# Optimization experiments

Measured on AMD Instinct MI355X. Metric: run time of the kernel, lower is better.

Reference implementation:

```python
import jax, jax.numpy as jnp
import numpy as np

NUM_CATEGORIES = 64
INPUT_DIM = 256
HIDDEN_DIM = 256
N = 4096  # number of samples (each with its own category)
M = 16    # rows per sample


def setup_inputs() -> dict:
    key = jax.random.key(0)
    k_x, k_cat, k_W = jax.random.split(key, 3)
    x = jax.random.normal(k_x, (N, M, INPUT_DIM), dtype=jnp.float32)
    cat_ids = jax.random.randint(k_cat, (N,), 0, NUM_CATEGORIES, dtype=jnp.int64)
    W = 0.02 * jax.random.normal(k_W, (NUM_CATEGORIES, INPUT_DIM, HIDDEN_DIM), dtype=jnp.float32)
    b = jnp.zeros((NUM_CATEGORIES, HIDDEN_DIM), dtype=jnp.float32)
    return {"x": x, "cat_ids": cat_ids, "W": W, "b": b}


def reference(x, cat_ids, W, b):
    # Gather per-sample weights/biases, then batched matmul + bias add.
    selected_W = W[cat_ids]              # [N, input_dim, hidden_dim]
    selected_b = b[cat_ids]              # [N, hidden_dim]
    out = jnp.einsum('nmi,nih->nmh', x, selected_W) + selected_b[:, None, :]
    return out
```

## Files before the change

### kernel.cpp

```cpp
#include <hip/hip_runtime.h>
#include <hip/hip_bf16.h>
#include <stdint.h>

#define N_SAMPLES 4096
#define M_ROWS 16
#define K_DIM 256
#define H_DIM 256
#define N_CATS 64
#define SPB 4
#define MAX_PADDED (N_SAMPLES + N_CATS * (SPB - 1))
#define NGROUP (MAX_PADDED / SPB)
#define GPX (NGROUP / 8)
#define GEMM_GRID (NGROUP * 2)

typedef _Float16 half8 __attribute__((ext_vector_type(8)));
typedef float floatx4 __attribute__((ext_vector_type(4)));

#define WT_BYTES ((size_t)N_CATS * K_DIM * H_DIM * 2)
#define ORD_OFF  WT_BYTES
#define WS_NEED  (ORD_OFF + (size_t)MAX_PADDED * 4)

__global__ __launch_bounds__(256)
void prep_combined(const float* __restrict__ W, _Float16* __restrict__ Wt,
                   const int* __restrict__ cat, int* __restrict__ ord) {
  const int tid = threadIdx.x;
  if (blockIdx.x < 1024) {
    __shared__ _Float16 t[64][72];
    const int bid = blockIdx.x;
    const int c  = bid >> 4;
    const int kb = (bid >> 2) & 3;
    const int hb = bid & 3;
    const int r  = tid >> 2;
    const int cg = (tid & 3) * 16;
    const float* src = W + ((size_t)c << 16) + (size_t)(kb * 64 + r) * 256 + hb * 64 + cg;
#pragma unroll
    for (int j = 0; j < 16; j += 4) {
      float4 v = *(const float4*)(src + j);
      t[r][cg + j + 0] = (_Float16)v.x;
      t[r][cg + j + 1] = (_Float16)v.y;
      t[r][cg + j + 2] = (_Float16)v.z;
      t[r][cg + j + 3] = (_Float16)v.w;
    }
    __syncthreads();
    _Float16* dst = Wt + ((size_t)c << 16) + (size_t)(hb * 64 + r) * 256 + kb * 64 + cg;
    half8 o0, o1;
#pragma unroll
    for (int j = 0; j < 8; j++) o0[j] = t[cg + j][r];
#pragma unroll
    for (int j = 0; j < 8; j++) o1[j] = t[cg + 8 + j][r];
    *(half8*)(dst) = o0;
    *(half8*)(dst + 8) = o1;
  } else {
    __shared__ int hist[N_CATS];
    __shared__ int poffs[N_CATS];
    __shared__ int curs[N_CATS];
    if (tid < N_CATS) hist[tid] = 0;
    for (int i = tid; i < MAX_PADDED; i += 256) ord[i] = -1;
    __syncthreads();
    for (int i = tid; i < N_SAMPLES; i += 256) atomicAdd(&hist[cat[i]], 1);
    __syncthreads();
    if (tid == 0) {
      int run = 0;
      for (int c = 0; c < N_CATS; c++) {
        poffs[c] = run;
        run += ((hist[c] + SPB - 1) / SPB) * SPB;
      }
    }
    if (tid < N_CATS) curs[tid] = 0;
    __syncthreads();
    for (int i = tid; i < N_SAMPLES; i += 256) {
      int c = cat[i];
      int p = poffs[c] + atomicAdd(&curs[c], 1);
      ord[p] = i;
    }
  }
}

__global__ __launch_bounds__(256, 8)
void gemm_kernel(const float* __restrict__ x, const int* __restrict__ cat_ids,
                 const float* __restrict__ bias, const _Float16* __restrict__ Wt,
                 const int* __restrict__ ord, float* __restrict__ out) {
  __shared__ _Float16 sA[64 * 32];
  __shared__ _Float16 sB[128 * 32];
  __shared__ int s_meta[SPB];

  const int tid = threadIdx.x;
  const int B = blockIdx.x;
  const int xcd = B & 7;
  const int slot = B >> 3;
  const int h_half = slot & 1;
  const int group = xcd * GPX + (slot >> 1);
  const int h0 = h_half << 7;

  if (tid < SPB) s_meta[tid] = ord[group * SPB + tid];
  __syncthreads();
  const int s0 = s_meta[0];
  if (s0 < 0) return;
  const int cat = cat_ids[s0];

  const int wid  = tid >> 6;
  const int lane = tid & 63;
  const int l15  = lane & 15;
  const int quad = lane >> 4;

  const int arow = tid >> 2;
  const int akq  = tid & 3;
  const int asmp = s_meta[arow >> 4];
  const float* asrc = (asmp >= 0)
      ? (x + ((size_t)asmp * 16 + (arow & 15)) * K_DIM + akq * 8) : nullptr;
  _Float16* adst = &sA[arow * 32 + akq * 8];

  const _Float16* wbase = Wt + ((size_t)cat << 16);

  floatx4 acc[4][2];
#pragma unroll
  for (int i = 0; i < 4; i++)
#pragma unroll
    for (int j = 0; j < 2; j++)
#pragma unroll
      for (int e = 0; e < 4; e++) acc[i][j][e] = 0.0f;

  for (int kt = 0; kt < K_DIM / 32; ++kt) {
    __syncthreads();
    if (asrc) {
      const float4* p = (const float4*)(asrc + kt * 32);
      float4 v0 = p[0], v1 = p[1];
      half8 h;
      h[0] = (_Float16)v0.x; h[1] = (_Float16)v0.y;
      h[2] = (_Float16)v0.z; h[3] = (_Float16)v0.w;
      h[4] = (_Float16)v1.x; h[5] = (_Float16)v1.y;
      h[6] = (_Float16)v1.z; h[7] = (_Float16)v1.w;
      *(half8*)adst = h;
    } else {
      half8 h;
#pragma unroll
      for (int j = 0; j < 8; j++) h[j] = (_Float16)0.0f;
      *(half8*)adst = h;
    }
#pragma unroll
    for (int j = 0; j < 2; j++) {
      const int hloc = wid * 16 + 64 * j;
      const _Float16* g = wbase + (size_t)(h0 + hloc + (lane >> 2)) * K_DIM + kt * 32 + (lane & 3) * 8;
      __builtin_amdgcn_global_load_lds(
          (__attribute__((address_space(1))) void*)g,
          (__attribute__((address_space(3))) void*)&sB[hloc * 32], 16, 0, 0);
    }
    __syncthreads();
    half8 af[4], bf[2];
#pragma unroll
    for (int mt = 0; mt < 4; mt++)
      af[mt] = *(const half8*)&sA[(mt * 16 + l15) * 32 + quad * 8];
#pragma unroll
    for (int nt = 0; nt < 2; nt++)
      bf[nt] = *(const half8*)&sB[(wid * 32 + nt * 16 + l15) * 32 + quad * 8];
#pragma unroll
    for (int mt = 0; mt < 4; mt++)
#pragma unroll
      for (int nt = 0; nt < 2; nt++)
        acc[mt][nt] = __builtin_amdgcn_mfma_f32_16x16x32_f16(af[mt], bf[nt], acc[mt][nt], 0, 0, 0);
  }

#pragma unroll
  for (int mt = 0; mt < 4; mt++) {
    int s = s_meta[mt];
    if (s < 0) continue;
    float* obase = out + (size_t)s * 16 * H_DIM;
#pragma unroll
    for (int nt = 0; nt < 2; nt++) {
      int col = h0 + wid * 32 + nt * 16 + l15;
      float bv = bias[cat * H_DIM + col];
#pragma unroll
      for (int r = 0; r < 4; r++) {
        int row = quad * 4 + r;
        obase[(size_t)row * H_DIM + col] = acc[mt][nt][r] + bv;
      }
    }
  }
}

__global__ __launch_bounds__(256)
void naive_kernel(const float* __restrict__ x, const int* __restrict__ cat,
                  const float* __restrict__ W, const float* __restrict__ bias,
                  float* __restrict__ out) {
  __shared__ float sx[16 * 256];
  const int n = blockIdx.x;
  const int tid = threadIdx.x;
  const int c = cat[n];
  const float* xs = x + (size_t)n * 16 * 256;
  for (int i = tid; i < 16 * 256; i += 256) sx[i] = xs[i];
  __syncthreads();
  const float* Wc = W + ((size_t)c << 16);
  float accv[16];
  float bv = bias[c * 256 + tid];
#pragma unroll
  for (int m = 0; m < 16; m++) accv[m] = bv;
  for (int k = 0; k < 256; k++) {
    float w = Wc[(size_t)k * 256 + tid];
#pragma unroll
    for (int m = 0; m < 16; m++) accv[m] += sx[m * 256 + k] * w;
  }
#pragma unroll
  for (int m = 0; m < 16; m++) out[((size_t)n * 16 + m) * 256 + tid] = accv[m];
}

extern "C" void kernel_launch(void* const* d_in, const int* in_sizes, int n_in,
                              void* d_out, int out_size, void* d_ws, size_t ws_size,
                              hipStream_t stream) {
  const float* x    = (const float*)d_in[0];
  const int*   cat  = (const int*)d_in[1];
  const float* W    = (const float*)d_in[2];
  const float* bias = (const float*)d_in[3];
  float* out = (float*)d_out;

  if (ws_size < WS_NEED) {
    naive_kernel<<<N_SAMPLES, 256, 0, stream>>>(x, cat, W, bias, out);
    return;
  }

  char* ws = (char*)d_ws;
  _Float16* Wt = (_Float16*)ws;
  int* ord = (int*)(ws + ORD_OFF);

  prep_combined<<<1025, 256, 0, stream>>>(W, Wt, cat, ord);
  gemm_kernel<<<GEMM_GRID, 256, 0, stream>>>(x, cat, bias, Wt, ord, out);
}
```

Measured before the change: 176.6 us.

## Stage full-K A tile in LDS and load B fragments directly to registers

Replaces the 8-step K loop, which had two barriers per step, with a single upfront load. The whole 64x256 fp16 A tile goes into padded LDS (row stride 264) with all x loads in flight at once. Each wave loads its B fragments for all K straight from global into registers, dropping the B LDS staging. Only one barrier remains before the MFMA loop. In exchange it uses more LDS and registers (launch bounds lowered to 4 waves per SIMD), so occupancy may fall.

Result: faster. 169.5 us (-4.0%).

```diff
diff --git a/kernel.cpp b/kernel.cpp
--- a/kernel.cpp
+++ b/kernel.cpp
@@ -12,6 +12,7 @@
 #define NGROUP (MAX_PADDED / SPB)
 #define GPX (NGROUP / 8)
 #define GEMM_GRID (NGROUP * 2)
+#define AROW_STRIDE 264
 
 typedef _Float16 half8 __attribute__((ext_vector_type(8)));
 typedef float floatx4 __attribute__((ext_vector_type(4)));
@@ -76,12 +77,11 @@
   }
 }
 
-__global__ __launch_bounds__(256, 8)
+__global__ __launch_bounds__(256, 4)
 void gemm_kernel(const float* __restrict__ x, const int* __restrict__ cat_ids,
                  const float* __restrict__ bias, const _Float16* __restrict__ Wt,
                  const int* __restrict__ ord, float* __restrict__ out) {
-  __shared__ _Float16 sA[64 * 32];
-  __shared__ _Float16 sB[128 * 32];
+  __shared__ _Float16 sA[64 * AROW_STRIDE];
   __shared__ int s_meta[SPB];
 
   const int tid = threadIdx.x;
@@ -103,14 +103,43 @@
   const int l15  = lane & 15;
   const int quad = lane >> 4;
 
-  const int arow = tid >> 2;
-  const int akq  = tid & 3;
-  const int asmp = s_meta[arow >> 4];
-  const float* asrc = (asmp >= 0)
-      ? (x + ((size_t)asmp * 16 + (arow & 15)) * K_DIM + akq * 8) : nullptr;
-  _Float16* adst = &sA[arow * 32 + akq * 8];
+  const int r = tid >> 2;
+  const int q = tid & 3;
+  const int smp = s_meta[r >> 4];
+  const float* asrc = (smp >= 0)
+      ? (x + ((size_t)smp * 16 + (r & 15)) * K_DIM + q * 64) : nullptr;
+  _Float16* adst = &sA[r * AROW_STRIDE];
+
+#pragma unroll
+  for (int hf = 0; hf < 2; hf++) {
+    float4 v[8];
+    if (asrc) {
+#pragma unroll
+      for (int j = 0; j < 8; j++) v[j] = ((const float4*)asrc)[hf * 8 + j];
+    } else {
+#pragma unroll
+      for (int j = 0; j < 8; j++) v[j] = make_float4(0.f, 0.f, 0.f, 0.f);
+    }
+#pragma unroll
+    for (int oj = 0; oj < 4; oj++) {
+      half8 h;
+      h[0] = (_Float16)v[oj * 2].x;     h[1] = (_Float16)v[oj * 2].y;
+      h[2] = (_Float16)v[oj * 2].z;     h[3] = (_Float16)v[oj * 2].w;
+      h[4] = (_Float16)v[oj * 2 + 1].x; h[5] = (_Float16)v[oj * 2 + 1].y;
+      h[6] = (_Float16)v[oj * 2 + 1].z; h[7] = (_Float16)v[oj * 2 + 1].w;
+      *(half8*)&adst[(q * 8 + hf * 4 + oj) * 8] = h;
+    }
+  }
 
   const _Float16* wbase = Wt + ((size_t)cat << 16);
+  half8 bf[8][2];
+#pragma unroll
+  for (int kt = 0; kt < 8; kt++)
+#pragma unroll
+    for (int nt = 0; nt < 2; nt++) {
+      const int col = h0 + wid * 32 + nt * 16 + l15;
+      bf[kt][nt] = *(const half8*)(wbase + (size_t)col * K_DIM + kt * 32 + quad * 8);
+    }
 
   floatx4 acc[4][2];
 #pragma unroll
@@ -120,46 +149,25 @@
 #pragma unroll
       for (int e = 0; e < 4; e++) acc[i][j][e] = 0.0f;
 
-  for (int kt = 0; kt < K_DIM / 32; ++kt) {
-    __syncthreads();
-    if (asrc) {
-      const float4* p = (const float4*)(asrc + kt * 32);
-      float4 v0 = p[0], v1 = p[1];
-      half8 h;
-      h[0] = (_Float16)v0.x; h[1] = (_Float16)v0.y;
-      h[2] = (_Float16)v0.z; h[3] = (_Float16)v0.w;
-      h[4] = (_Float16)v1.x; h[5] = (_Float16)v1.y;
-      h[6] = (_Float16)v1.z; h[7] = (_Float16)v1.w;
-      *(half8*)adst = h;
-    } else {
-      half8 h;
-#pragma unroll
-      for (int j = 0; j < 8; j++) h[j] = (_Float16)0.0f;
-      *(half8*)adst = h;
-    }
-#pragma unroll
-    for (int j = 0; j < 2; j++) {
-      const int hloc = wid * 16 + 64 * j;
-      const _Float16* g = wbase + (size_t)(h0 + hloc + (lane >> 2)) * K_DIM + kt * 32 + (lane & 3) * 8;
-      __builtin_amdgcn_global_load_lds(
-          (__attribute__((address_space(1))) void*)g,
-          (__attribute__((address_space(3))) void*)&sB[hloc * 32], 16, 0, 0);
-    }
-    __syncthreads();
-    half8 af[4], bf[2];
+  __syncthreads();
+
+#pragma unroll
+  for (int kt = 0; kt < 8; kt++) {
+    half8 af[4];
 #pragma unroll
     for (int mt = 0; mt < 4; mt++)
-      af[mt] = *(const half8*)&sA[(mt * 16 + l15) * 32 + quad * 8];
-#pragma unroll
-    for (int nt = 0; nt < 2; nt++)
-      bf[nt] = *(const half8*)&sB[(wid * 32 + nt * 16 + l15) * 32 + quad * 8];
+      af[mt] = *(const half8*)&sA[(mt * 16 + l15) * AROW_STRIDE + (kt * 4 + quad) * 8];
 #pragma unroll
     for (int mt = 0; mt < 4; mt++)
 #pragma unroll
       for (int nt = 0; nt < 2; nt++)
-        acc[mt][nt] = __builtin_amdgcn_mfma_f32_16x16x32_f16(af[mt], bf[nt], acc[mt][nt], 0, 0, 0);
-  }
-
+        acc[mt][nt] = __builtin_amdgcn_mfma_f32_16x16x32_f16(af[mt], bf[kt][nt], acc[mt][nt], 0, 0, 0);
+  }
+
+  float bv[2];
+#pragma unroll
+  for (int nt = 0; nt < 2; nt++)
+    bv[nt] = bias[cat * H_DIM + h0 + wid * 32 + nt * 16 + l15];
 #pragma unroll
   for (int mt = 0; mt < 4; mt++) {
     int s = s_meta[mt];
@@ -168,11 +176,10 @@
 #pragma unroll
     for (int nt = 0; nt < 2; nt++) {
       int col = h0 + wid * 32 + nt * 16 + l15;
-      float bv = bias[cat * H_DIM + col];
-#pragma unroll
-      for (int r = 0; r < 4; r++) {
-        int row = quad * 4 + r;
-        obase[(size_t)row * H_DIM + col] = acc[mt][nt][r] + bv;
+#pragma unroll
+      for (int rr = 0; rr < 4; rr++) {
+        int row = quad * 4 + rr;
+        obase[(size_t)row * H_DIM + col] = acc[mt][nt][rr] + bv[nt];
       }
     }
   }
```
